# Performance work log

Hardware: AMD Instinct MI355X
Metric: run time of the kernel (lower is better)

## Reference

```python
import jax, jax.numpy as jnp
import numpy as np

EPS = 1e-5

def _dwconv(x, w, pad):
    # x: [N,C,H,W], w: [C,1,K,K] depthwise (feature_group_count=C)
    return jax.lax.conv_general_dilated(
        x, w, window_strides=(1, 1), padding=[(pad, pad), (pad, pad)],
        dimension_numbers=('NCHW', 'OIHW', 'NCHW'),
        feature_group_count=w.shape[0])

def _bn(y, gamma, beta, mean, var):
    scale = (gamma / jnp.sqrt(var + EPS))[None, :, None, None]
    shift = (beta - mean * gamma / jnp.sqrt(var + EPS))[None, :, None, None]
    return y * scale + shift

def setup_inputs() -> dict:
    key = jax.random.key(0)
    ks = jax.random.split(key, 12)
    C, K, SK = 384, 31, 5
    x = jax.random.normal(ks[0], (16, C, 56, 56), jnp.float32)
    lk_w = jax.random.normal(ks[1], (C, 1, K, K), jnp.float32) * 0.05
    sk_w = jax.random.normal(ks[2], (C, 1, SK, SK), jnp.float32) * 0.2
    return {
        'x': x,
        'lk_w': lk_w,
        'lk_gamma': jax.random.uniform(ks[3], (C,), jnp.float32, 0.5, 1.5),
        'lk_beta': jax.random.normal(ks[4], (C,), jnp.float32) * 0.1,
        'lk_mean': jax.random.normal(ks[5], (C,), jnp.float32) * 0.1,
        'lk_var': jax.random.uniform(ks[6], (C,), jnp.float32, 0.5, 1.5),
        'sk_w': sk_w,
        'sk_gamma': jax.random.uniform(ks[7], (C,), jnp.float32, 0.5, 1.5),
        'sk_beta': jax.random.normal(ks[8], (C,), jnp.float32) * 0.1,
        'sk_mean': jax.random.normal(ks[9], (C,), jnp.float32) * 0.1,
        'sk_var': jax.random.uniform(ks[10], (C,), jnp.float32, 0.5, 1.5),
    }

def reference(x, lk_w, lk_gamma, lk_beta, lk_mean, lk_var,
              sk_w, sk_gamma, sk_beta, sk_mean, sk_var):
    K = lk_w.shape[-1]   # 31
    SK = sk_w.shape[-1]  # 5
    out = _bn(_dwconv(x, lk_w, K // 2), lk_gamma, lk_beta, lk_mean, lk_var)
    out = out + _bn(_dwconv(x, sk_w, SK // 2), sk_gamma, sk_beta, sk_mean, sk_var)
    return out
```

## Files before the change

### kernel.cpp

```cpp
#include <hip/hip_runtime.h>
#include <cstdint>
#include <cstddef>

#define C_CH  384
#define HW    56
#define PLANE 3136
#define KK    31
#define PAD   15

typedef _Float16 f16x8 __attribute__((ext_vector_type(8)));
typedef float    f32x16 __attribute__((ext_vector_type(16)));
typedef uint32_t u32x4 __attribute__((ext_vector_type(4)));
typedef uint64_t u64x2 __attribute__((ext_vector_type(2)));

#define ROWB   256
#define NROWS  94
#define PLSZ   (NROWS*ROWB)
#define WE_OFF (2*PLSZ)
#define WO_OFF (WE_OFF + 31*192)
#define LDS_BYTES (WO_OFF + 31*192)

static __device__ __forceinline__ uint32_t pack_h2(float a, float b) {
    return __builtin_bit_cast(uint32_t, __builtin_amdgcn_cvt_pkrtz(a, b));
}

__global__ void prep_weights(const float* __restrict__ lk_w,
                             const float* __restrict__ lk_g, const float* __restrict__ lk_b,
                             const float* __restrict__ lk_m, const float* __restrict__ lk_v,
                             const float* __restrict__ sk_w,
                             const float* __restrict__ sk_g, const float* __restrict__ sk_b,
                             const float* __restrict__ sk_m, const float* __restrict__ sk_v,
                             float* __restrict__ wm, float* __restrict__ bias) {
    const int c = blockIdx.x;
    const float s1 = lk_g[c] / sqrtf(lk_v[c] + 1e-5f);
    const float s2 = sk_g[c] / sqrtf(sk_v[c] + 1e-5f);
    if (threadIdx.x == 0)
        bias[c] = (lk_b[c] - lk_m[c] * s1) + (sk_b[c] - sk_m[c] * s2);
    for (int i = threadIdx.x; i < KK * 32; i += blockDim.x) {
        const int ky = i >> 5, kx = i & 31;
        float w = 0.f;
        if (kx < KK) {
            w = lk_w[c * (KK*KK) + ky * KK + kx] * s1;
            if (ky >= 13 && ky <= 17 && kx >= 13 && kx <= 17)
                w += sk_w[c * 25 + (ky - 13) * 5 + (kx - 13)] * s2;
        }
        wm[c * (KK*32) + i] = w;
    }
}

__global__ __launch_bounds__(256, 2) void dw31_mfma(const float* __restrict__ x,
                                                    const float* __restrict__ wm,
                                                    const float* __restrict__ bias,
                                                    float* __restrict__ out) {
    __shared__ __align__(16) uint8_t lds8[LDS_BYTES];
    const int c  = blockIdx.x;
    const int ng = blockIdx.y;
    const int tid = threadIdx.x;
    const int wid = tid >> 6, lane = tid & 63;
    const int wt = wid & 1, hp = wid >> 1;
    const int col = lane & 31, hi = lane >> 5;

    {
        uint4 z = make_uint4(0u,0u,0u,0u);
        uint4* p = (uint4*)lds8;
        for (int i = tid; i < LDS_BYTES/16; i += 256) p[i] = z;
    }
    __syncthreads();

    for (int i = tid; i < 2*784; i += 256) {
        const int nn = (i >= 784);
        const int ii = i - nn*784;
        const int r = ii / 14, q = ii - r*14;
        const float4 v = ((const float4*)(x + ((size_t)((ng*2+nn)*C_CH + c))*PLANE))[ii];
        const int rl = r + PAD;
        int byte0 = nn*PLSZ + rl*ROWB + 2*(16 + 4*q);
        byte0 ^= (rl & 14) << 3;
        uint2 h;
        h.x = pack_h2(v.x, v.y);
        h.y = pack_h2(v.z, v.w);
        *(uint2*)(lds8 + byte0) = h;
    }
    {
        const float* wrow = wm + c*(KK*32);
        for (int idx = tid; idx < 2*961; idx += 256) {
            const int cp = (idx >= 961);
            const int r2 = idx - cp*961;
            const int ky = r2 / 31, kx = r2 - ky*31;
            const int t = kx + (cp ? 31 : 32);
            const int byte0 = (cp ? WO_OFF : WE_OFF) + ky*192 + 2*t;
            *(_Float16*)(lds8 + byte0) = (_Float16)wrow[ky*32 + kx];
        }
    }
    __syncthreads();

    f32x16 acc0 = {0.f}; f32x16 acc1 = {0.f};
    const int m    = col;
    const int nn_a = m >> 4, hr = m & 15;
    const int h0a  = (hp*2 + 0) * 16;
    const int h0b  = (hp*2 + 1) * 16;
    const int acolbyte = 2*(wt*32 + 8*hi);

    for (int ky = 0; ky < KK; ++ky) {
        f16x8 bf[4];
        #pragma unroll
        for (int cc = 0; cc < 4; ++cc) {
            const int t0 = 16*cc + 8*hi + 31 - col;
            const int off = (t0 & 1) ? (WO_OFF + ((t0 - 1) << 1))
                                     : (WE_OFF + (t0 << 1));
            const uint32_t* wp = (const uint32_t*)(lds8 + ky*192 + off);
            u32x4 u = { wp[0], wp[1], wp[2], wp[3] };
            bf[cc] = __builtin_bit_cast(f16x8, u);
        }
        {
            const int rl = h0a + hr + ky;
            const int sw = (rl & 14) << 3;
            const int base = nn_a*PLSZ + rl*ROWB + acolbyte;
            #pragma unroll
            for (int cc = 0; cc < 4; ++cc) {
                u64x2 u = *(const u64x2*)(lds8 + ((base + 32*cc) ^ sw));
                acc0 = __builtin_amdgcn_mfma_f32_32x32x16_f16(
                    __builtin_bit_cast(f16x8, u), bf[cc], acc0, 0, 0, 0);
            }
        }
        {
            const int rl = h0b + hr + ky;
            const int sw = (rl & 14) << 3;
            const int base = nn_a*PLSZ + rl*ROWB + acolbyte;
            #pragma unroll
            for (int cc = 0; cc < 4; ++cc) {
                u64x2 u = *(const u64x2*)(lds8 + ((base + 32*cc) ^ sw));
                acc1 = __builtin_amdgcn_mfma_f32_32x32x16_f16(
                    __builtin_bit_cast(f16x8, u), bf[cc], acc1, 0, 0, 0);
            }
        }
    }

    const float b = bias[c];
    const int w = wt*32 + col;
    if (w < HW) {
        #pragma unroll
        for (int t = 0; t < 2; ++t) {
            const int h0 = t ? h0b : h0a;
            #pragma unroll
            for (int reg = 0; reg < 16; ++reg) {
                const int mm = (reg & 3) + 8*(reg >> 2) + 4*hi;
                const int nn = mm >> 4, hro = mm & 15;
                const int h = h0 + hro;
                if (h < HW) {
                    const float v = (t ? acc1[reg] : acc0[reg]) + b;
                    out[((size_t)((ng*2+nn)*C_CH + c))*PLANE + h*HW + w] = v;
                }
            }
        }
    }
}

extern "C" void kernel_launch(void* const* d_in, const int* in_sizes, int n_in,
                              void* d_out, int out_size, void* d_ws, size_t ws_size,
                              hipStream_t stream) {
    const float* x    = (const float*)d_in[0];
    const float* lk_w = (const float*)d_in[1];
    const float* lk_g = (const float*)d_in[2];
    const float* lk_b = (const float*)d_in[3];
    const float* lk_m = (const float*)d_in[4];
    const float* lk_v = (const float*)d_in[5];
    const float* sk_w = (const float*)d_in[6];
    const float* sk_g = (const float*)d_in[7];
    const float* sk_b = (const float*)d_in[8];
    const float* sk_m = (const float*)d_in[9];
    const float* sk_v = (const float*)d_in[10];
    float* out = (float*)d_out;

    float* wm   = (float*)d_ws;
    float* bias = wm + C_CH * (KK * 32);

    prep_weights<<<C_CH, 256, 0, stream>>>(lk_w, lk_g, lk_b, lk_m, lk_v,
                                           sk_w, sk_g, sk_b, sk_m, sk_v,
                                           wm, bias);

    dim3 grid(C_CH, 8);
    dw31_mfma<<<grid, 256, 0, stream>>>(x, wm, bias, out);
}
```

Baseline: 247.6 us.

## Precompute per-lane MFMA weight fragments in global memory and reuse A-loads across tiles

Adds a prep kernel that builds a per-channel, per-ky, per-lane table of f16 Toeplitz weight fragments in the workspace. The main kernel streams these fragments from global memory, prefetching one ky ahead, instead of staging weights in LDS. Each wave now covers both width halves for a 16-row band, so six shared A-fragment LDS loads feed eight MFMAs per ky. This cuts LDS traffic and the LDS footprint, at the cost of an extra kernel launch and a table of about 46 MB that must be read through cache. The old LDS-weight path is kept as a fallback when the workspace is too small.

After: 284.1 us. 1.15x slower.

```diff
diff --git a/kernel.cpp b/kernel.cpp
--- a/kernel.cpp
+++ b/kernel.cpp
@@ -16,6 +16,7 @@
 #define ROWB   256
 #define NROWS  94
 #define PLSZ   (NROWS*ROWB)
+#define LDSG   (2*PLSZ)
 #define WE_OFF (2*PLSZ)
 #define WO_OFF (WE_OFF + 31*192)
 #define LDS_BYTES (WO_OFF + 31*192)
@@ -48,10 +49,114 @@
     }
 }
 
-__global__ __launch_bounds__(256, 2) void dw31_mfma(const float* __restrict__ x,
-                                                    const float* __restrict__ wm,
-                                                    const float* __restrict__ bias,
-                                                    float* __restrict__ out) {
+__global__ void prep_frags(const float* __restrict__ wm, u32x4* __restrict__ btab) {
+    const int c = blockIdx.x, tid = threadIdx.x;
+    const int cc = tid >> 6, lane = tid & 63;
+    const int hi = lane >> 5, col = lane & 31;
+    const int s0 = 16*cc + 8*hi + 31 - col - 32;
+    const float* wr = wm + c * (KK*32);
+    for (int ky = 0; ky < KK; ++ky) {
+        f16x8 f;
+        #pragma unroll
+        for (int e = 0; e < 8; ++e) {
+            const int idx = s0 + e;
+            const float v = (idx >= 0 && idx < KK) ? wr[ky*32 + idx] : 0.f;
+            f[e] = (_Float16)v;
+        }
+        btab[((size_t)c*KK + ky)*256 + tid] = __builtin_bit_cast(u32x4, f);
+    }
+}
+
+__global__ __launch_bounds__(256, 2) void dw31_mfma_g(const float* __restrict__ x,
+                                                      const u32x4* __restrict__ btab,
+                                                      const float* __restrict__ bias,
+                                                      float* __restrict__ out) {
+    __shared__ __align__(16) uint8_t lds8[LDSG];
+    const int c = blockIdx.x, ng = blockIdx.y;
+    const int tid = threadIdx.x, hp = tid >> 6, lane = tid & 63;
+    const int col = lane & 31, hi = lane >> 5;
+
+    {
+        uint4 z = make_uint4(0u,0u,0u,0u);
+        uint4* p = (uint4*)lds8;
+        for (int i = tid; i < LDSG/16; i += 256) p[i] = z;
+    }
+    __syncthreads();
+    for (int i = tid; i < 2*784; i += 256) {
+        const int nn = (i >= 784);
+        const int ii = i - nn*784;
+        const int r = ii / 14, q = ii - r*14;
+        const float4 v = ((const float4*)(x + ((size_t)((ng*2+nn)*C_CH + c))*PLANE))[ii];
+        const int rl = r + PAD;
+        int byte0 = nn*PLSZ + rl*ROWB + 2*(16 + 4*q);
+        byte0 ^= (rl & 14) << 3;
+        uint2 h;
+        h.x = pack_h2(v.x, v.y);
+        h.y = pack_h2(v.z, v.w);
+        *(uint2*)(lds8 + byte0) = h;
+    }
+    __syncthreads();
+
+    const int nn_a = col >> 4, hr = col & 15, h0 = hp * 16;
+    const u32x4* bt = btab + (size_t)c*KK*256 + lane;
+
+    f32x16 acc0 = {0.f}, acc1 = {0.f};
+    u32x4 b0 = bt[0], b1 = bt[64], b2 = bt[128], b3 = bt[192];
+
+    #pragma unroll 1
+    for (int ky = 0; ky < KK; ++ky) {
+        const int kyn = (ky < KK-1) ? ky + 1 : ky;
+        const u32x4* btn = bt + kyn*256;
+        u32x4 n0 = btn[0], n1 = btn[64], n2 = btn[128], n3 = btn[192];
+
+        const int rl = h0 + hr + ky;
+        const int sw = (rl & 14) << 3;
+        const int base = nn_a*PLSZ + rl*ROWB + 16*hi;
+        u64x2 a0 = *(const u64x2*)(lds8 + ((base      ) ^ sw));
+        u64x2 a1 = *(const u64x2*)(lds8 + ((base +  32) ^ sw));
+        u64x2 a2 = *(const u64x2*)(lds8 + ((base +  64) ^ sw));
+        u64x2 a3 = *(const u64x2*)(lds8 + ((base +  96) ^ sw));
+        u64x2 a4 = *(const u64x2*)(lds8 + ((base + 128) ^ sw));
+        u64x2 a5 = *(const u64x2*)(lds8 + ((base + 160) ^ sw));
+
+        acc0 = __builtin_amdgcn_mfma_f32_32x32x16_f16(
+            __builtin_bit_cast(f16x8, a0), __builtin_bit_cast(f16x8, b0), acc0, 0, 0, 0);
+        acc1 = __builtin_amdgcn_mfma_f32_32x32x16_f16(
+            __builtin_bit_cast(f16x8, a2), __builtin_bit_cast(f16x8, b0), acc1, 0, 0, 0);
+        acc0 = __builtin_amdgcn_mfma_f32_32x32x16_f16(
+            __builtin_bit_cast(f16x8, a1), __builtin_bit_cast(f16x8, b1), acc0, 0, 0, 0);
+        acc1 = __builtin_amdgcn_mfma_f32_32x32x16_f16(
+            __builtin_bit_cast(f16x8, a3), __builtin_bit_cast(f16x8, b1), acc1, 0, 0, 0);
+        acc0 = __builtin_amdgcn_mfma_f32_32x32x16_f16(
+            __builtin_bit_cast(f16x8, a2), __builtin_bit_cast(f16x8, b2), acc0, 0, 0, 0);
+        acc1 = __builtin_amdgcn_mfma_f32_32x32x16_f16(
+            __builtin_bit_cast(f16x8, a4), __builtin_bit_cast(f16x8, b2), acc1, 0, 0, 0);
+        acc0 = __builtin_amdgcn_mfma_f32_32x32x16_f16(
+            __builtin_bit_cast(f16x8, a3), __builtin_bit_cast(f16x8, b3), acc0, 0, 0, 0);
+        acc1 = __builtin_amdgcn_mfma_f32_32x32x16_f16(
+            __builtin_bit_cast(f16x8, a5), __builtin_bit_cast(f16x8, b3), acc1, 0, 0, 0);
+
+        b0 = n0; b1 = n1; b2 = n2; b3 = n3;
+    }
+
+    const float bsv = bias[c];
+    #pragma unroll
+    for (int reg = 0; reg < 16; ++reg) {
+        const int mm = (reg & 3) + 8*(reg >> 2) + 4*hi;
+        const int nn = mm >> 4, hro = mm & 15;
+        const int h = h0 + hro;
+        if (h < HW) {
+            float* op = out + ((size_t)((ng*2+nn)*C_CH + c))*PLANE + h*HW;
+            op[col] = acc0[reg] + bsv;
+            if (col < 24) op[32 + col] = acc1[reg] + bsv;
+        }
+    }
+}
+
+__global__ __launch_bounds__(256, 2) void dw31_mfma_l(const float* __restrict__ x,
+                                                      const float* __restrict__ wm,
+                                                      const float* __restrict__ bias,
+                                                      float* __restrict__ out) {
     __shared__ __align__(16) uint8_t lds8[LDS_BYTES];
     const int c  = blockIdx.x;
     const int ng = blockIdx.y;
@@ -66,7 +171,6 @@
         for (int i = tid; i < LDS_BYTES/16; i += 256) p[i] = z;
     }
     __syncthreads();
-
     for (int i = tid; i < 2*784; i += 256) {
         const int nn = (i >= 784);
         const int ii = i - nn*784;
@@ -171,13 +275,24 @@
     const float* sk_v = (const float*)d_in[10];
     float* out = (float*)d_out;
 
-    float* wm   = (float*)d_ws;
-    float* bias = wm + C_CH * (KK * 32);
-
-    prep_weights<<<C_CH, 256, 0, stream>>>(lk_w, lk_g, lk_b, lk_m, lk_v,
-                                           sk_w, sk_g, sk_b, sk_m, sk_v,
-                                           wm, bias);
+    const size_t table_bytes = (size_t)C_CH * KK * 256 * 16;
+    const size_t wm_floats   = (size_t)C_CH * KK * 32;
+    const size_t need_g      = table_bytes + (wm_floats + C_CH) * sizeof(float);
 
     dim3 grid(C_CH, 8);
-    dw31_mfma<<<grid, 256, 0, stream>>>(x, wm, bias, out);
-}
+    if (ws_size >= need_g) {
+        u32x4* btab = (u32x4*)d_ws;
+        float* wm   = (float*)((uint8_t*)d_ws + table_bytes);
+        float* bias = wm + wm_floats;
+        prep_weights<<<C_CH, 256, 0, stream>>>(lk_w, lk_g, lk_b, lk_m, lk_v,
+                                               sk_w, sk_g, sk_b, sk_m, sk_v, wm, bias);
+        prep_frags<<<C_CH, 256, 0, stream>>>(wm, btab);
+        dw31_mfma_g<<<grid, 256, 0, stream>>>(x, btab, bias, out);
+    } else {
+        float* wm   = (float*)d_ws;
+        float* bias = wm + wm_floats;
+        prep_weights<<<C_CH, 256, 0, stream>>>(lk_w, lk_g, lk_b, lk_m, lk_v,
+                                               sk_w, sk_g, sk_b, sk_m, sk_v, wm, bias);
+        dw31_mfma_l<<<grid, 256, 0, stream>>>(x, wm, bias, out);
+    }
+}
```
